# Kernel optimization log

Hardware: AMD Instinct MI355X
Metric: run time of the kernel (lower is better)

## Reference

```python
import jax, jax.numpy as jnp
import numpy as np

DIM = 64        # feature channels of x
HEADS = 4
POS_DIM = 3
NUM_IDS = 8
STR_IN = 512    # strength_linear input size
B, S, W = 4, 1024, 8   # batch, sequence (S1), source-views (S2)


def setup_inputs() -> dict:
    key = jax.random.key(0)
    ks = jax.random.split(key, 18)
    stdv = 1.0 / np.sqrt(DIM * DIM)  # embedding init per module
    d8 = DIM // 8
    u = lambda k, shp, s: jax.random.uniform(k, shp, jnp.float32, -s, s)
    return {
        "x": jax.random.normal(ks[0], (B, DIM, S, W), jnp.float32),
        "pos": jax.random.normal(ks[1], (B, S, POS_DIM), jnp.float32),
        "strength": jax.random.normal(ks[2], (STR_IN,), jnp.float32),
        "embed_id1": 3,
        "q_emb_w": u(ks[3], (NUM_IDS, DIM * DIM), stdv),
        "k_emb_w": u(ks[4], (NUM_IDS, DIM * DIM), stdv),
        "v_emb_w": u(ks[5], (NUM_IDS, DIM * DIM), stdv),
        "pos_w1": u(ks[6], (POS_DIM, POS_DIM), 1.0 / np.sqrt(POS_DIM)),
        "pos_b1": u(ks[7], (POS_DIM,), 1.0 / np.sqrt(POS_DIM)),
        "pos_w2": u(ks[8], (d8, POS_DIM), 1.0 / np.sqrt(POS_DIM)),
        "pos_b2": u(ks[9], (d8,), 1.0 / np.sqrt(POS_DIM)),
        "head_w": u(ks[10], (HEADS, d8), 1.0 / np.sqrt(d8)),
        "head_b": u(ks[11], (HEADS,), 1.0 / np.sqrt(d8)),
        "gate": jnp.ones((HEADS,), jnp.float32),
        "out_w": u(ks[12], (DIM, DIM), 1.0 / np.sqrt(DIM)),
        "out_b": u(ks[13], (DIM,), 1.0 / np.sqrt(DIM)),
        "str_w": u(ks[14], (DIM, STR_IN), 1.0 / np.sqrt(STR_IN)),
        "str_b": u(ks[15], (DIM,), 1.0 / np.sqrt(STR_IN)),
    }


def reference(x, pos, strength, embed_id1, q_emb_w, k_emb_w, v_emb_w,
              pos_w1, pos_b1, pos_w2, pos_b2, head_w, head_b, gate,
              out_w, out_b, str_w, str_b):
    # strength projection: Linear(512, dim)
    s = strength @ str_w.T + str_b                    # [dim]
    xt = jnp.transpose(x, (0, 2, 3, 1))               # [B, S, W, dim]
    qe = q_emb_w[embed_id1].reshape(DIM, DIM)
    ke = k_emb_w[embed_id1].reshape(DIM, DIM)
    ve = v_emb_w[embed_id1].reshape(DIM, DIM)

    def proj(emb):
        y = xt @ emb.T + s                            # [B, S, W, dim]
        # collapse (W, dim) -> (heads, head_dim), heads to axis 1
        y = y.reshape(B, S, HEADS, -1)
        return jnp.transpose(y, (0, 2, 1, 3))         # [B, H, S, hd]

    q, k, v = proj(qe), proj(ke), proj(ve)
    hd = q.shape[-1]
    attn = jax.nn.softmax(jnp.einsum("bhsd,bhtd->bhst", q, k) / np.sqrt(hd), axis=-1)

    # relative-position attention branch
    ph = jax.nn.relu(pos @ pos_w1.T + pos_b1) @ pos_w2.T + pos_b2   # [B, S, dim//8]
    diff = ph[:, :, None, :] - ph[:, None, :, :]                    # [B, S, S, dim//8]
    pos_attn = jnp.transpose(diff @ head_w.T + head_b, (0, 3, 1, 2))
    pos_attn = jax.nn.softmax(pos_attn, axis=-1)                    # [B, H, S, S]

    g = jax.nn.sigmoid(gate).reshape(1, -1, 1, 1)
    attn = (1.0 - g) * attn + g * pos_attn
    attn = attn / jnp.sum(attn, axis=-1, keepdims=True)

    out = jnp.einsum("bhst,bhtd->bhsd", attn, v)      # [B, H, S, hd]
    out = jnp.transpose(out, (0, 2, 1, 3)).reshape(B, S, W, DIM)
    return out @ out_w.T + out_b                      # [B, S, W, dim]
```

## Files before the change

kernel.cpp:

```cpp
#include <hip/hip_runtime.h>
#include <math.h>
#include <stdint.h>

#define B_ 4
#define S_ 1024
#define F_ 512
#define HD 128
#define SOFT_C 4.0f

typedef __attribute__((ext_vector_type(8))) short short8;
typedef __attribute__((ext_vector_type(4))) float f32x4;
typedef __attribute__((ext_vector_type(4))) unsigned int u32x4;
typedef __attribute__((ext_vector_type(2))) unsigned int u32x2;

__device__ __forceinline__ unsigned short f2bf(float f) {
    unsigned int u = __float_as_uint(f);
    u = (u + 0x7FFFu + ((u >> 16) & 1u)) >> 16;
    return (unsigned short)u;
}
__device__ __forceinline__ float bf2f(unsigned int s) {
    return __uint_as_float(s << 16);
}
__device__ __forceinline__ void pack_hilo(const float* v, u32x4& hi, u32x4& lo) {
    #pragma unroll
    for (int p = 0; p < 4; ++p) {
        unsigned int h0 = f2bf(v[2 * p]), h1 = f2bf(v[2 * p + 1]);
        float l0 = v[2 * p] - bf2f(h0), l1 = v[2 * p + 1] - bf2f(h1);
        hi[p] = h0 | (h1 << 16);
        lo[p] = (unsigned int)f2bf(l0) | ((unsigned int)f2bf(l1) << 16);
    }
}

__global__ __launch_bounds__(256) void k_qkv(
    const float* __restrict__ x, const int* __restrict__ embed_id,
    const float* __restrict__ qw, const float* __restrict__ kw,
    const float* __restrict__ vw,
    const float* __restrict__ strength, const float* __restrict__ str_w,
    const float* __restrict__ str_b,
    const float* __restrict__ pos, const float* __restrict__ pw1,
    const float* __restrict__ pb1, const float* __restrict__ pw2,
    const float* __restrict__ pb2, const float* __restrict__ head_w,
    unsigned short* __restrict__ yqh, unsigned short* __restrict__ ykh,
    unsigned short* __restrict__ yvt2,
    float* __restrict__ sv_g, float* __restrict__ xbar)
{
    __shared__ unsigned short whi[3][4096];
    __shared__ unsigned short wlo[3][4096];
    __shared__ float part_s[4][64];
    __shared__ float sv_s[64], svq_s[64];
    __shared__ float xr_s[4][8];
    __shared__ float red_s[4][4];
    __shared__ float inv_s[4];

    const int tid  = threadIdx.x;
    const int wv   = tid >> 6;
    const int lane = tid & 63;
    const int quad = lane >> 4;
    const int l15  = lane & 15;
    const float SCALE = 0.08838834764831845f;

    if (blockIdx.x >= 512) {
        const int bi = blockIdx.x - 512;
        const int b = bi >> 6, c = bi & 63;
        float w1_[9], b1_[3], w2_[24], b2_[8], hw_[32];
        #pragma unroll
        for (int i = 0; i < 9; ++i)  w1_[i] = pw1[i];
        #pragma unroll
        for (int i = 0; i < 3; ++i)  b1_[i] = pb1[i];
        #pragma unroll
        for (int i = 0; i < 24; ++i) w2_[i] = pw2[i];
        #pragma unroll
        for (int i = 0; i < 8; ++i)  b2_[i] = pb2[i];
        #pragma unroll
        for (int i = 0; i < 32; ++i) hw_[i] = head_w[i];

        float pv_[4][4];
        float ps[4] = {0.f, 0.f, 0.f, 0.f};
        #pragma unroll
        for (int rr = 0; rr < 4; ++rr) {
            const int s = tid * 4 + rr;
            float p0 = pos[(b * S_ + s) * 3 + 0];
            float p1 = pos[(b * S_ + s) * 3 + 1];
            float p2 = pos[(b * S_ + s) * 3 + 2];
            float h0 = fmaxf(0.f, p0 * w1_[0] + p1 * w1_[1] + p2 * w1_[2] + b1_[0]);
            float h1 = fmaxf(0.f, p0 * w1_[3] + p1 * w1_[4] + p2 * w1_[5] + b1_[1]);
            float h2 = fmaxf(0.f, p0 * w1_[6] + p1 * w1_[7] + p2 * w1_[8] + b1_[2]);
            float ph[8];
            #pragma unroll
            for (int o8 = 0; o8 < 8; ++o8)
                ph[o8] = h0 * w2_[o8 * 3] + h1 * w2_[o8 * 3 + 1]
                       + h2 * w2_[o8 * 3 + 2] + b2_[o8];
            #pragma unroll
            for (int h = 0; h < 4; ++h) {
                float A = 0.f;
                #pragma unroll
                for (int o8 = 0; o8 < 8; ++o8) A += ph[o8] * hw_[h * 8 + o8];
                pv_[rr][h] = __expf(-A - 1.0f);
                ps[h] += pv_[rr][h];
            }
        }
        #pragma unroll
        for (int h = 0; h < 4; ++h)
            #pragma unroll
            for (int off = 1; off < 64; off <<= 1)
                ps[h] += __shfl_xor(ps[h], off);
        if (lane == 0)
            #pragma unroll
            for (int h = 0; h < 4; ++h) red_s[wv][h] = ps[h];
        __syncthreads();
        if (tid < 4)
            inv_s[tid] = 1.f / (red_s[0][tid] + red_s[1][tid]
                              + red_s[2][tid] + red_s[3][tid]);
        __syncthreads();

        const float* xc = x + (size_t)b * 524288 + c * 8192;
        float acc[8] = {};
        #pragma unroll
        for (int rr = 0; rr < 4; ++rr) {
            const int s = tid * 4 + rr;
            f32x4 x0 = *(const f32x4*)(xc + s * 8);
            f32x4 x1 = *(const f32x4*)(xc + s * 8 + 4);
            float q0 = pv_[rr][0] * inv_s[0];
            float q1 = pv_[rr][1] * inv_s[1];
            float q2 = pv_[rr][2] * inv_s[2];
            float q3 = pv_[rr][3] * inv_s[3];
            acc[0] += q0 * x0[0]; acc[1] += q0 * x0[1];
            acc[2] += q1 * x0[2]; acc[3] += q1 * x0[3];
            acc[4] += q2 * x1[0]; acc[5] += q2 * x1[1];
            acc[6] += q3 * x1[2]; acc[7] += q3 * x1[3];
        }
        #pragma unroll
        for (int j = 0; j < 8; ++j)
            #pragma unroll
            for (int off = 1; off < 64; off <<= 1)
                acc[j] += __shfl_xor(acc[j], off);
        if (lane == 0)
            #pragma unroll
            for (int j = 0; j < 8; ++j) xr_s[wv][j] = acc[j];
        __syncthreads();
        if (tid < 8)
            xbar[(b * 8 + tid) * 64 + c] = xr_s[0][tid] + xr_s[1][tid]
                                         + xr_s[2][tid] + xr_s[3][tid];
        return;
    }

    const int id = embed_id[0];
    #pragma unroll
    for (int m = 0; m < 3; ++m) {
        const float* src = (m == 0 ? qw : m == 1 ? kw : vw) + id * 4096;
        const float sc = (m == 0) ? SCALE : 1.0f;
        for (int i = tid; i < 4096; i += 256) {
            float v = src[i] * sc;
            unsigned short hh = f2bf(v);
            const int r = i >> 6, cc = i & 63;
            const int off = ((r >> 4) * 2 + (cc >> 5)) * 512
                          + ((cc >> 3) & 3) * 128 + (r & 15) * 8 + (cc & 7);
            whi[m][off] = hh;
            wlo[m][off] = f2bf(v - bf2f(hh));
        }
    }
    {
        const float* wrow = str_w + lane * 512 + wv * 128;
        const float* st   = strength + wv * 128;
        float a = 0.f;
        #pragma unroll
        for (int j4 = 0; j4 < 32; ++j4) {
            f32x4 wv4 = *(const f32x4*)(wrow + j4 * 4);
            f32x4 s4  = *(const f32x4*)(st + j4 * 4);
            a += wv4[0] * s4[0] + wv4[1] * s4[1] + wv4[2] * s4[2] + wv4[3] * s4[3];
        }
        part_s[wv][lane] = a;
    }
    __syncthreads();
    if (tid < 64) {
        float v = part_s[0][tid] + part_s[1][tid] + part_s[2][tid]
                + part_s[3][tid] + str_b[tid];
        sv_s[tid]  = v;
        svq_s[tid] = v * SCALE;
        if (blockIdx.x == 0) sv_g[tid] = v;
    }
    __syncthreads();

    const int r0   = blockIdx.x * 64 + wv * 16;
    const int b    = r0 >> 13;
    const int rloc = (r0 & 8191) + l15;
    const float* xb = x + (size_t)b * 524288;

    u32x4 xhi[2], xlo[2];
    #pragma unroll
    for (int kc = 0; kc < 2; ++kc) {
        float xv[8];
        #pragma unroll
        for (int j = 0; j < 8; ++j)
            xv[j] = xb[(kc * 32 + quad * 8 + j) * 8192 + rloc];
        pack_hilo(xv, xhi[kc], xlo[kc]);
    }

    float svq_l[4], sv_l[4];
    #pragma unroll
    for (int nt = 0; nt < 4; ++nt) {
        svq_l[nt] = svq_s[nt * 16 + l15];
        sv_l[nt]  = sv_s[nt * 16 + l15];
    }
    f32x4 svA[4];
    #pragma unroll
    for (int mt = 0; mt < 4; ++mt)
        svA[mt] = *(const f32x4*)&sv_s[mt * 16 + quad * 4];

    int idxq[4];
    #pragma unroll
    for (int rr = 0; rr < 4; ++rr) {
        const int rl = quad * 4 + rr;
        const int w_ = rl & 7;
        const int s_loc = ((r0 & 8191) >> 3) + (rl >> 3);
        idxq[rr] = (b * 4 + (w_ >> 1)) * 131072 + s_loc * 128 + (w_ & 1) * 64 + l15;
    }

    const int row_g = r0 + l15;
    const int s_idx = (row_g >> 3) & 1023;
    const int w_idx = row_g & 7;
    const int bh    = b * 4 + (w_idx >> 1);
    const int dbase = (w_idx & 1) * 64;
    unsigned short* vtb = yvt2 + (size_t)bh * 131072 + (s_idx >> 6) * 8192
                        + (size_t)dbase * 64 + (s_idx & 63);

    #pragma unroll
    for (int mat = 0; mat < 2; ++mat) {
        const unsigned short* mh = whi[mat];
        const unsigned short* ml = wlo[mat];
        f32x4 acc[4] = {};
        #pragma unroll
        for (int kc = 0; kc < 2; ++kc)
            #pragma unroll
            for (int nt = 0; nt < 4; ++nt) {
                const int off = (nt * 2 + kc) * 512 + quad * 128 + l15 * 8;
                u32x4 ehi = *(const u32x4*)(mh + off);
                u32x4 elo = *(const u32x4*)(ml + off);
                acc[nt] = __builtin_amdgcn_mfma_f32_16x16x32_bf16(
                    __builtin_bit_cast(short8, xhi[kc]),
                    __builtin_bit_cast(short8, ehi), acc[nt], 0, 0, 0);
                acc[nt] = __builtin_amdgcn_mfma_f32_16x16x32_bf16(
                    __builtin_bit_cast(short8, xlo[kc]),
                    __builtin_bit_cast(short8, ehi), acc[nt], 0, 0, 0);
                acc[nt] = __builtin_amdgcn_mfma_f32_16x16x32_bf16(
                    __builtin_bit_cast(short8, xhi[kc]),
                    __builtin_bit_cast(short8, elo), acc[nt], 0, 0, 0);
            }
        unsigned short* y = (mat == 0 ? yqh : ykh);
        const float* svp = (mat == 0 ? svq_l : sv_l);
        #pragma unroll
        for (int nt = 0; nt < 4; ++nt)
            #pragma unroll
            for (int rr = 0; rr < 4; ++rr)
                y[(size_t)idxq[rr] + nt * 16] = f2bf(acc[nt][rr] + svp[nt]);
    }

    {
        const unsigned short* mh = whi[2];
        const unsigned short* ml = wlo[2];
        f32x4 acc[4] = {};
        #pragma unroll
        for (int kc = 0; kc < 2; ++kc)
            #pragma unroll
            for (int mt = 0; mt < 4; ++mt) {
                const int off = (mt * 2 + kc) * 512 + quad * 128 + l15 * 8;
                u32x4 ehi = *(const u32x4*)(mh + off);
                u32x4 elo = *(const u32x4*)(ml + off);
                acc[mt] = __builtin_amdgcn_mfma_f32_16x16x32_bf16(
                    __builtin_bit_cast(short8, ehi),
                    __builtin_bit_cast(short8, xhi[kc]), acc[mt], 0, 0, 0);
                acc[mt] = __builtin_amdgcn_mfma_f32_16x16x32_bf16(
                    __builtin_bit_cast(short8, ehi),
                    __builtin_bit_cast(short8, xlo[kc]), acc[mt], 0, 0, 0);
                acc[mt] = __builtin_amdgcn_mfma_f32_16x16x32_bf16(
                    __builtin_bit_cast(short8, elo),
                    __builtin_bit_cast(short8, xhi[kc]), acc[mt], 0, 0, 0);
            }
        #pragma unroll
        for (int mt = 0; mt < 4; ++mt)
            #pragma unroll
            for (int rr = 0; rr < 4; ++rr) {
                const int c = mt * 16 + quad * 4 + rr;
                vtb[(size_t)c * 64] = f2bf(acc[mt][rr] + svA[mt][rr]);
            }
    }
}

__global__ __launch_bounds__(256, 2) void k_attn(
    const unsigned short* __restrict__ yqh, const unsigned short* __restrict__ ykh,
    const unsigned short* __restrict__ yvt2,
    const float* __restrict__ xbar, const float* __restrict__ vw,
    const int* __restrict__ embed_id, const float* __restrict__ sv,
    const float* __restrict__ gate,
    const float* __restrict__ out_w, const float* __restrict__ out_b,
    float* __restrict__ out)
{
    __shared__ __align__(16) unsigned short kx[2][64 * 136];
    __shared__ __align__(16) unsigned short vx[2][128 * 72];
    __shared__ float vbar_s[128];
    __shared__ float vbarP_s[128];
    __shared__ float lsq_s[2][2][16];

    const int tid  = threadIdx.x;
    const int w    = tid >> 6;
    const int lane = tid & 63;
    const int quad = lane >> 4;
    const int l15  = lane & 15;
    const int bh = blockIdx.x & 15, qt = blockIdx.x >> 4;
    const int b = bh >> 2, h = bh & 3;
    const int s0 = qt * 32;
    const int qh = w >> 1;
    const int ts = w & 1;

    const unsigned short* ykb = ykh + (size_t)bh * 131072;
    const unsigned short* yvb = yvt2 + (size_t)bh * 131072;

    if (tid < 128) {
        const int c = tid & 63, wloc = tid >> 6;
        const float* ver = vw + embed_id[0] * 4096 + c * 64;
        const float* xbr = xbar + (b * 8 + h * 2 + wloc) * 64;
        float a = sv[c];
        #pragma unroll
        for (int j4 = 0; j4 < 16; ++j4) {
            f32x4 e4 = *(const f32x4*)(ver + j4 * 4);
            f32x4 x4 = *(const f32x4*)(xbr + j4 * 4);
            a += e4[0] * x4[0] + e4[1] * x4[1] + e4[2] * x4[2] + e4[3] * x4[3];
        }
        vbar_s[wloc * 64 + c] = a;
    }

    u32x4 qf[4];
    #pragma unroll
    for (int kc = 0; kc < 4; ++kc)
        qf[kc] = *(const u32x4*)(yqh + (size_t)bh * 131072
                 + (s0 + qh * 16 + l15) * 128 + kc * 32 + quad * 8);

    #pragma unroll
    for (int r = 0; r < 4; ++r) {
        const int off = r * 2048 + tid * 8;
        *(u32x4*)&kx[0][(off >> 7) * 136 + (off & 127)] =
            *(const u32x4*)(ykb + off);
        *(u32x4*)&vx[0][(off >> 6) * 72 + (off & 63)] =
            *(const u32x4*)(yvb + off);
    }
    __syncthreads();

    if (tid < 128) {
        const int seg = tid >> 6, dq = tid & 63;
        const float* wr = out_w + dq * 64;
        float a = 0.f;
        #pragma unroll
        for (int j4 = 0; j4 < 16; ++j4) {
            f32x4 w4 = *(const f32x4*)(wr + j4 * 4);
            f32x4 v4 = *(const f32x4*)&vbar_s[seg * 64 + j4 * 4];
            a += w4[0] * v4[0] + w4[1] * v4[1] + w4[2] * v4[2] + w4[3] * v4[3];
        }
        vbarP_s[seg * 64 + dq] = a;
    }

    f32x4 o[8] = {};
    float lsum = 0.f;
    const int srcA = ((quad & 1) << 5) + l15;

    for (int it = 0; it < 16; ++it) {
        const int cur = it & 1;
        u32x4 kst[4], vst[4];
        const bool pre = (it < 15);
        if (pre) {
            const unsigned short* ksrc = ykb + (it + 1) * 8192;
            const unsigned short* vsrc = yvb + (it + 1) * 8192;
            #pragma unroll
            for (int r = 0; r < 4; ++r)
                kst[r] = *(const u32x4*)(ksrc + r * 2048 + tid * 8);
            #pragma unroll
            for (int r = 0; r < 4; ++r)
                vst[r] = *(const u32x4*)(vsrc + r * 2048 + tid * 8);
        }

        const unsigned short* kxc = kx[cur];
        const unsigned short* vxc = vx[cur];

        f32x4 sa0 = {}, sa1 = {};
        #pragma unroll
        for (int kc = 0; kc < 4; ++kc) {
            u32x4 a0 = *(const u32x4*)&kxc[(ts * 32 + l15) * 136 + kc * 32 + quad * 8];
            sa0 = __builtin_amdgcn_mfma_f32_16x16x32_bf16(
                __builtin_bit_cast(short8, a0),
                __builtin_bit_cast(short8, qf[kc]), sa0, 0, 0, 0);
        }
        #pragma unroll
        for (int kc = 0; kc < 4; ++kc) {
            u32x4 a1 = *(const u32x4*)&kxc[(ts * 32 + 16 + l15) * 136 + kc * 32 + quad * 8];
            sa1 = __builtin_amdgcn_mfma_f32_16x16x32_bf16(
                __builtin_bit_cast(short8, a1),
                __builtin_bit_cast(short8, qf[kc]), sa1, 0, 0, 0);
        }

        float p0[4], p1[4];
        #pragma unroll
        for (int r = 0; r < 4; ++r) {
            p0[r] = __expf(sa0[r] - SOFT_C);
            p1[r] = __expf(sa1[r] - SOFT_C);
            lsum += p0[r] + p1[r];
        }

        unsigned int pk00 = (unsigned int)f2bf(p0[0]) | ((unsigned int)f2bf(p0[1]) << 16);
        unsigned int pk01 = (unsigned int)f2bf(p0[2]) | ((unsigned int)f2bf(p0[3]) << 16);
        unsigned int pk10 = (unsigned int)f2bf(p1[0]) | ((unsigned int)f2bf(p1[1]) << 16);
        unsigned int pk11 = (unsigned int)f2bf(p1[2]) | ((unsigned int)f2bf(p1[3]) << 16);
        unsigned int sel0 = (quad < 2) ? pk00 : pk10;
        unsigned int sel1 = (quad < 2) ? pk01 : pk11;
        u32x4 pf;
        pf[0] = (unsigned int)__shfl((int)sel0, srcA);
        pf[1] = (unsigned int)__shfl((int)sel1, srcA);
        pf[2] = (unsigned int)__shfl((int)sel0, srcA + 16);
        pf[3] = (unsigned int)__shfl((int)sel1, srcA + 16);

        #pragma unroll
        for (int dt = 0; dt < 8; ++dt) {
            u32x4 vf = *(const u32x4*)&vxc[(dt * 16 + l15) * 72 + ts * 32 + quad * 8];
            o[dt] = __builtin_amdgcn_mfma_f32_16x16x32_bf16(
                __builtin_bit_cast(short8, vf),
                __builtin_bit_cast(short8, pf), o[dt], 0, 0, 0);
        }

        if (pre) {
            #pragma unroll
            for (int r = 0; r < 4; ++r) {
                const int off = r * 2048 + tid * 8;
                *(u32x4*)&kx[cur ^ 1][(off >> 7) * 136 + (off & 127)] = kst[r];
            }
            #pragma unroll
            for (int r = 0; r < 4; ++r) {
                const int off = r * 2048 + tid * 8;
                *(u32x4*)&vx[cur ^ 1][(off >> 6) * 72 + (off & 63)] = vst[r];
            }
        }
        __syncthreads();
    }

    float* obuf = (float*)&kx[0][0];
    {
        float* ow_ = obuf + ((qh * 2 + ts) * 16 + l15) * 132;
        #pragma unroll
        for (int dt = 0; dt < 8; ++dt)
            *(f32x4*)(ow_ + dt * 16 + quad * 4) = o[dt];
    }
    lsum += __shfl_xor(lsum, 16);
    lsum += __shfl_xor(lsum, 32);
    if (quad == 0) lsq_s[qh][ts][l15] = lsum;
    __syncthreads();

    const float gf = 1.f / (1.f + __expf(-gate[h]));
    const float cf = (1.f - gf) / (lsq_s[qh][0][l15] + lsq_s[qh][1][l15]);
    const float* oa  = obuf + ((qh * 2 + 0) * 16 + l15) * 132;
    const float* obp = obuf + ((qh * 2 + 1) * 16 + l15) * 132;

    u32x4 bhi[2], blo[2];
    #pragma unroll
    for (int kc = 0; kc < 2; ++kc) {
        const int off = ts * 64 + kc * 32 + quad * 8;
        f32x4 a0 = *(const f32x4*)(oa + off);
        f32x4 a1 = *(const f32x4*)(oa + off + 4);
        f32x4 c0 = *(const f32x4*)(obp + off);
        f32x4 c1 = *(const f32x4*)(obp + off + 4);
        float yv[8] = {cf * (a0[0] + c0[0]), cf * (a0[1] + c0[1]),
                       cf * (a0[2] + c0[2]), cf * (a0[3] + c0[3]),
                       cf * (a1[0] + c1[0]), cf * (a1[1] + c1[1]),
                       cf * (a1[2] + c1[2]), cf * (a1[3] + c1[3])};
        pack_hilo(yv, bhi[kc], blo[kc]);
    }

    f32x4 acc[4] = {};
    #pragma unroll
    for (int kc = 0; kc < 2; ++kc)
        #pragma unroll
        for (int mt = 0; mt < 4; ++mt) {
            const float* wsrc2 = out_w + (mt * 16 + l15) * 64 + kc * 32 + quad * 8;
            f32x4 w0 = *(const f32x4*)wsrc2;
            f32x4 w1 = *(const f32x4*)(wsrc2 + 4);
            float wv8[8] = {w0[0], w0[1], w0[2], w0[3], w1[0], w1[1], w1[2], w1[3]};
            u32x4 ahi, alo;
            pack_hilo(wv8, ahi, alo);
            acc[mt] = __builtin_amdgcn_mfma_f32_16x16x32_bf16(
                __builtin_bit_cast(short8, ahi),
                __builtin_bit_cast(short8, bhi[kc]), acc[mt], 0, 0, 0);
            acc[mt] = __builtin_amdgcn_mfma_f32_16x16x32_bf16(
                __builtin_bit_cast(short8, ahi),
                __builtin_bit_cast(short8, blo[kc]), acc[mt], 0, 0, 0);
            acc[mt] = __builtin_amdgcn_mfma_f32_16x16x32_bf16(
                __builtin_bit_cast(short8, alo),
                __builtin_bit_cast(short8, bhi[kc]), acc[mt], 0, 0, 0);
        }

    const int w_seg = h * 2 + ts;
    const size_t rowb = ((size_t)(b * S_ + s0 + qh * 16 + l15) * 8 + w_seg) * 64;
    #pragma unroll
    for (int mt = 0; mt < 4; ++mt) {
        f32x4 vb   = *(const f32x4*)&vbarP_s[ts * 64 + mt * 16 + quad * 4];
        f32x4 bias = *(const f32x4*)(out_b + mt * 16 + quad * 4);
        f32x4 res;
        #pragma unroll
        for (int j = 0; j < 4; ++j) res[j] = acc[mt][j] + gf * vb[j] + bias[j];
        *(f32x4*)(out + rowb + mt * 16 + quad * 4) = res;
    }
}

extern "C" void kernel_launch(void* const* d_in, const int* in_sizes, int n_in,
                              void* d_out, int out_size, void* d_ws, size_t ws_size,
                              hipStream_t stream) {
    (void)in_sizes; (void)n_in; (void)out_size; (void)ws_size;
    const float* x        = (const float*)d_in[0];
    const float* pos      = (const float*)d_in[1];
    const float* strength = (const float*)d_in[2];
    const int*   embed_id = (const int*)d_in[3];
    const float* qw       = (const float*)d_in[4];
    const float* kw       = (const float*)d_in[5];
    const float* vw       = (const float*)d_in[6];
    const float* pw1      = (const float*)d_in[7];
    const float* pb1      = (const float*)d_in[8];
    const float* pw2      = (const float*)d_in[9];
    const float* pb2      = (const float*)d_in[10];
    const float* head_w   = (const float*)d_in[11];
    const float* gate     = (const float*)d_in[13];
    const float* out_w    = (const float*)d_in[14];
    const float* out_b    = (const float*)d_in[15];
    const float* str_w    = (const float*)d_in[16];
    const float* str_b    = (const float*)d_in[17];
    float* out = (float*)d_out;

    unsigned short* yqh   = (unsigned short*)d_ws;
    unsigned short* ykh   = yqh + 2097152;
    unsigned short* yvt2  = ykh + 2097152;
    float* sv   = (float*)(yvt2 + 2097152);
    float* xbar = sv + 64;

    k_qkv<<<768, 256, 0, stream>>>(x, embed_id, qw, kw, vw,
                                   strength, str_w, str_b,
                                   pos, pw1, pb1, pw2, pb2, head_w,
                                   yqh, ykh, yvt2, sv, xbar);
    k_attn<<<512, 256, 0, stream>>>(yqh, ykh, yvt2, xbar, vw, embed_id, sv,
                                    gate, out_w, out_b, out);
}
```

Baseline: 144.0 us.

## Fuse QKV projection and attention into one cooperative kernel with grid sync

Merges the projection kernel and the attention kernel into a single cooperative launch of 512 blocks that synchronise with a grid barrier, removing one kernel launch and the gap between launches. The separate positional/xbar blocks are folded into the projection blocks: each block computes a half-sequence xbar partial, written to two buffers that are summed later. Weight hi/lo conversion is vectorised, and launch bounds now request two blocks per CU. If the cooperative launch fails it falls back to two ordinary launches with a mode flag. The cost is a grid-wide barrier, redundant recomputation of the positional softmax sums in every block, and a larger shared allocation.

```diff
diff --git a/kernel.cpp b/kernel.cpp
--- a/kernel.cpp
+++ b/kernel.cpp
@@ -1,6 +1,9 @@
 #include <hip/hip_runtime.h>
+#include <hip/hip_cooperative_groups.h>
 #include <math.h>
 #include <stdint.h>
+
+namespace cg = cooperative_groups;
 
 #define B_ 4
 #define S_ 1024
@@ -31,26 +34,22 @@
     }
 }
 
-__global__ __launch_bounds__(256) void k_qkv(
-    const float* __restrict__ x, const int* __restrict__ embed_id,
+__global__ __launch_bounds__(256, 2) void k_fused(
+    const float* __restrict__ x, const float* __restrict__ pos,
+    const float* __restrict__ strength, const int* __restrict__ embed_id,
     const float* __restrict__ qw, const float* __restrict__ kw,
     const float* __restrict__ vw,
-    const float* __restrict__ strength, const float* __restrict__ str_w,
-    const float* __restrict__ str_b,
-    const float* __restrict__ pos, const float* __restrict__ pw1,
-    const float* __restrict__ pb1, const float* __restrict__ pw2,
-    const float* __restrict__ pb2, const float* __restrict__ head_w,
+    const float* __restrict__ pw1, const float* __restrict__ pb1,
+    const float* __restrict__ pw2, const float* __restrict__ pb2,
+    const float* __restrict__ head_w, const float* __restrict__ gate,
+    const float* __restrict__ out_w, const float* __restrict__ out_b,
+    const float* __restrict__ str_w, const float* __restrict__ str_b,
     unsigned short* __restrict__ yqh, unsigned short* __restrict__ ykh,
     unsigned short* __restrict__ yvt2,
-    float* __restrict__ sv_g, float* __restrict__ xbar)
+    float* __restrict__ sv_g, float* __restrict__ xbar0,
+    float* __restrict__ xbar1, float* __restrict__ out, int mode)
 {
-    __shared__ unsigned short whi[3][4096];
-    __shared__ unsigned short wlo[3][4096];
-    __shared__ float part_s[4][64];
-    __shared__ float sv_s[64], svq_s[64];
-    __shared__ float xr_s[4][8];
-    __shared__ float red_s[4][4];
-    __shared__ float inv_s[4];
+    __shared__ __align__(16) unsigned char smem[72960];
 
     const int tid  = threadIdx.x;
     const int wv   = tid >> 6;
@@ -59,450 +58,469 @@
     const int l15  = lane & 15;
     const float SCALE = 0.08838834764831845f;
 
-    if (blockIdx.x >= 512) {
-        const int bi = blockIdx.x - 512;
-        const int b = bi >> 6, c = bi & 63;
-        float w1_[9], b1_[3], w2_[24], b2_[8], hw_[32];
+    if (mode != 2) {
+        unsigned short* whiB = (unsigned short*)smem;
+        unsigned short* wloB = whiB + 12288;
+        float* part_s = (float*)(smem + 49152);
+        float* sv_s   = (float*)(smem + 50176);
+        float* svq_s  = (float*)(smem + 50432);
+        float* xr_s   = (float*)(smem + 50688);
+        float* red_s  = (float*)(smem + 50816);
+        float* inv_s  = (float*)(smem + 50880);
+
+        const int id = embed_id[0];
+
+        for (int cc = tid; cc < 1536; cc += 256) {
+            const int m  = cc >> 9;
+            const int e0 = (cc & 511) << 3;
+            const float* src = (m == 0 ? qw : m == 1 ? kw : vw) + id * 4096 + e0;
+            const float sc = (m == 0) ? SCALE : 1.0f;
+            f32x4 a0 = *(const f32x4*)src;
+            f32x4 a1 = *(const f32x4*)(src + 4);
+            float v8[8] = {a0[0] * sc, a0[1] * sc, a0[2] * sc, a0[3] * sc,
+                           a1[0] * sc, a1[1] * sc, a1[2] * sc, a1[3] * sc};
+            u32x4 hi, lo;
+            pack_hilo(v8, hi, lo);
+            const int r = e0 >> 6, c = e0 & 63;
+            const int off = ((r >> 4) * 2 + (c >> 5)) * 512
+                          + ((c >> 3) & 3) * 128 + (r & 15) * 8;
+            *(u32x4*)(whiB + m * 4096 + off) = hi;
+            *(u32x4*)(wloB + m * 4096 + off) = lo;
+        }
+
+        {
+            const float* wrow = str_w + lane * 512 + wv * 128;
+            const float* st   = strength + wv * 128;
+            float a = 0.f;
+            #pragma unroll
+            for (int j4 = 0; j4 < 32; ++j4) {
+                f32x4 wv4 = *(const f32x4*)(wrow + j4 * 4);
+                f32x4 s4  = *(const f32x4*)(st + j4 * 4);
+                a += wv4[0] * s4[0] + wv4[1] * s4[1] + wv4[2] * s4[2] + wv4[3] * s4[3];
+            }
+            part_s[wv * 64 + lane] = a;
+        }
+        __syncthreads();
+        if (tid < 64) {
+            float v = part_s[tid] + part_s[64 + tid] + part_s[128 + tid]
+                    + part_s[192 + tid] + str_b[tid];
+            sv_s[tid]  = v;
+            svq_s[tid] = v * SCALE;
+            if (blockIdx.x == 0) sv_g[tid] = v;
+        }
+        __syncthreads();
+
+        {
+            const int r0   = blockIdx.x * 64 + wv * 16;
+            const int b    = r0 >> 13;
+            const int rloc = (r0 & 8191) + l15;
+            const float* xb = x + (size_t)b * 524288;
+
+            u32x4 xhi[2], xlo[2];
+            #pragma unroll
+            for (int kc = 0; kc < 2; ++kc) {
+                float xv[8];
+                #pragma unroll
+                for (int j = 0; j < 8; ++j)
+                    xv[j] = xb[(kc * 32 + quad * 8 + j) * 8192 + rloc];
+                pack_hilo(xv, xhi[kc], xlo[kc]);
+            }
+
+            float svq_l[4], sv_l[4];
+            #pragma unroll
+            for (int nt = 0; nt < 4; ++nt) {
+                svq_l[nt] = svq_s[nt * 16 + l15];
+                sv_l[nt]  = sv_s[nt * 16 + l15];
+            }
+            f32x4 svA[4];
+            #pragma unroll
+            for (int mt = 0; mt < 4; ++mt)
+                svA[mt] = *(const f32x4*)&sv_s[mt * 16 + quad * 4];
+
+            int idxq[4];
+            #pragma unroll
+            for (int rr = 0; rr < 4; ++rr) {
+                const int rl = quad * 4 + rr;
+                const int w_ = rl & 7;
+                const int s_loc = ((r0 & 8191) >> 3) + (rl >> 3);
+                idxq[rr] = (b * 4 + (w_ >> 1)) * 131072 + s_loc * 128 + (w_ & 1) * 64 + l15;
+            }
+
+            const int row_g = r0 + l15;
+            const int s_idx = (row_g >> 3) & 1023;
+            const int w_idx = row_g & 7;
+            const int bh    = b * 4 + (w_idx >> 1);
+            const int dbase = (w_idx & 1) * 64;
+            unsigned short* vtb = yvt2 + (size_t)bh * 131072 + (s_idx >> 6) * 8192
+                                + (size_t)dbase * 64 + (s_idx & 63);
+
+            #pragma unroll
+            for (int mat = 0; mat < 2; ++mat) {
+                const unsigned short* mh = whiB + mat * 4096;
+                const unsigned short* ml = wloB + mat * 4096;
+                f32x4 acc[4] = {};
+                #pragma unroll
+                for (int kc = 0; kc < 2; ++kc)
+                    #pragma unroll
+                    for (int nt = 0; nt < 4; ++nt) {
+                        const int off = (nt * 2 + kc) * 512 + quad * 128 + l15 * 8;
+                        u32x4 ehi = *(const u32x4*)(mh + off);
+                        u32x4 elo = *(const u32x4*)(ml + off);
+                        acc[nt] = __builtin_amdgcn_mfma_f32_16x16x32_bf16(
+                            __builtin_bit_cast(short8, xhi[kc]),
+                            __builtin_bit_cast(short8, ehi), acc[nt], 0, 0, 0);
+                        acc[nt] = __builtin_amdgcn_mfma_f32_16x16x32_bf16(
+                            __builtin_bit_cast(short8, xlo[kc]),
+                            __builtin_bit_cast(short8, ehi), acc[nt], 0, 0, 0);
+                        acc[nt] = __builtin_amdgcn_mfma_f32_16x16x32_bf16(
+                            __builtin_bit_cast(short8, xhi[kc]),
+                            __builtin_bit_cast(short8, elo), acc[nt], 0, 0, 0);
+                    }
+                unsigned short* y = (mat == 0 ? yqh : ykh);
+                const float* svp = (mat == 0 ? svq_l : sv_l);
+                #pragma unroll
+                for (int nt = 0; nt < 4; ++nt)
+                    #pragma unroll
+                    for (int rr = 0; rr < 4; ++rr)
+                        y[(size_t)idxq[rr] + nt * 16] = f2bf(acc[nt][rr] + svp[nt]);
+            }
+
+            {
+                const unsigned short* mh = whiB + 2 * 4096;
+                const unsigned short* ml = wloB + 2 * 4096;
+                f32x4 acc[4] = {};
+                #pragma unroll
+                for (int kc = 0; kc < 2; ++kc)
+                    #pragma unroll
+                    for (int mt = 0; mt < 4; ++mt) {
+                        const int off = (mt * 2 + kc) * 512 + quad * 128 + l15 * 8;
+                        u32x4 ehi = *(const u32x4*)(mh + off);
+                        u32x4 elo = *(const u32x4*)(ml + off);
+                        acc[mt] = __builtin_amdgcn_mfma_f32_16x16x32_bf16(
+                            __builtin_bit_cast(short8, ehi),
+                            __builtin_bit_cast(short8, xhi[kc]), acc[mt], 0, 0, 0);
+                        acc[mt] = __builtin_amdgcn_mfma_f32_16x16x32_bf16(
+                            __builtin_bit_cast(short8, ehi),
+                            __builtin_bit_cast(short8, xlo[kc]), acc[mt], 0, 0, 0);
+                        acc[mt] = __builtin_amdgcn_mfma_f32_16x16x32_bf16(
+                            __builtin_bit_cast(short8, elo),
+                            __builtin_bit_cast(short8, xhi[kc]), acc[mt], 0, 0, 0);
+                    }
+                #pragma unroll
+                for (int mt = 0; mt < 4; ++mt)
+                    #pragma unroll
+                    for (int rr = 0; rr < 4; ++rr) {
+                        const int c = mt * 16 + quad * 4 + rr;
+                        vtb[(size_t)c * 64] = f2bf(acc[mt][rr] + svA[mt][rr]);
+                    }
+            }
+        }
+
+        {
+            const int g  = blockIdx.x;
+            const int xh = g >> 8, bi = g & 255;
+            const int bb = bi >> 6, c = bi & 63;
+
+            float w1_[9], b1_[3], w2_[24], b2_[8], hw_[32];
+            #pragma unroll
+            for (int i = 0; i < 9; ++i)  w1_[i] = pw1[i];
+            #pragma unroll
+            for (int i = 0; i < 3; ++i)  b1_[i] = pb1[i];
+            #pragma unroll
+            for (int i = 0; i < 24; ++i) w2_[i] = pw2[i];
+            #pragma unroll
+            for (int i = 0; i < 8; ++i)  b2_[i] = pb2[i];
+            #pragma unroll
+            for (int i = 0; i < 32; ++i) hw_[i] = head_w[i];
+
+            float evh[2][4];
+            float ps[4] = {0.f, 0.f, 0.f, 0.f};
+            #pragma unroll
+            for (int k = 0; k < 4; ++k) {
+                const int s = k * 256 + tid;
+                float p0 = pos[(bb * S_ + s) * 3 + 0];
+                float p1 = pos[(bb * S_ + s) * 3 + 1];
+                float p2 = pos[(bb * S_ + s) * 3 + 2];
+                float h0 = fmaxf(0.f, p0 * w1_[0] + p1 * w1_[1] + p2 * w1_[2] + b1_[0]);
+                float h1 = fmaxf(0.f, p0 * w1_[3] + p1 * w1_[4] + p2 * w1_[5] + b1_[1]);
+                float h2 = fmaxf(0.f, p0 * w1_[6] + p1 * w1_[7] + p2 * w1_[8] + b1_[2]);
+                float ph[8];
+                #pragma unroll
+                for (int o8 = 0; o8 < 8; ++o8)
+                    ph[o8] = h0 * w2_[o8 * 3] + h1 * w2_[o8 * 3 + 1]
+                           + h2 * w2_[o8 * 3 + 2] + b2_[o8];
+                #pragma unroll
+                for (int h = 0; h < 4; ++h) {
+                    float A = 0.f;
+                    #pragma unroll
+                    for (int o8 = 0; o8 < 8; ++o8) A += ph[o8] * hw_[h * 8 + o8];
+                    float e = __expf(-A - 1.0f);
+                    ps[h] += e;
+                    if ((k >> 1) == xh) evh[k & 1][h] = e;
+                }
+            }
+            #pragma unroll
+            for (int h = 0; h < 4; ++h)
+                #pragma unroll
+                for (int off = 1; off < 64; off <<= 1)
+                    ps[h] += __shfl_xor(ps[h], off);
+            if (lane == 0)
+                #pragma unroll
+                for (int h = 0; h < 4; ++h) red_s[wv * 4 + h] = ps[h];
+            __syncthreads();
+            if (tid < 4)
+                inv_s[tid] = 1.f / (red_s[tid] + red_s[4 + tid]
+                                  + red_s[8 + tid] + red_s[12 + tid]);
+            __syncthreads();
+
+            const float* xc = x + (size_t)bb * 524288 + c * 8192;
+            float acc[8] = {};
+            #pragma unroll
+            for (int kk = 0; kk < 2; ++kk) {
+                const int s = (xh * 2 + kk) * 256 + tid;
+                f32x4 x0 = *(const f32x4*)(xc + s * 8);
+                f32x4 x1 = *(const f32x4*)(xc + s * 8 + 4);
+                float q0 = evh[kk][0] * inv_s[0];
+                float q1 = evh[kk][1] * inv_s[1];
+                float q2 = evh[kk][2] * inv_s[2];
+                float q3 = evh[kk][3] * inv_s[3];
+                acc[0] += q0 * x0[0]; acc[1] += q0 * x0[1];
+                acc[2] += q1 * x0[2]; acc[3] += q1 * x0[3];
+                acc[4] += q2 * x1[0]; acc[5] += q2 * x1[1];
+                acc[6] += q3 * x1[2]; acc[7] += q3 * x1[3];
+            }
+            #pragma unroll
+            for (int j = 0; j < 8; ++j)
+                #pragma unroll
+                for (int off = 1; off < 64; off <<= 1)
+                    acc[j] += __shfl_xor(acc[j], off);
+            if (lane == 0)
+                #pragma unroll
+                for (int j = 0; j < 8; ++j) xr_s[wv * 8 + j] = acc[j];
+            __syncthreads();
+            if (tid < 8) {
+                float* xb_h = xh ? xbar1 : xbar0;
+                xb_h[(bb * 8 + tid) * 64 + c] = xr_s[tid] + xr_s[8 + tid]
+                                              + xr_s[16 + tid] + xr_s[24 + tid];
+            }
+        }
+
+        if (mode == 1) return;
+        __threadfence();
+        cg::this_grid().sync();
+    }
+
+    {
+        unsigned short* kxb = (unsigned short*)smem;
+        unsigned short* vxb = (unsigned short*)(smem + 34816);
+        float* vbar_s  = (float*)(smem + 71680);
+        float* vbarP_s = (float*)(smem + 72192);
+        float* lsq_s   = (float*)(smem + 72704);
+
+        const int bh = blockIdx.x & 15, qt = blockIdx.x >> 4;
+        const int b = bh >> 2, h = bh & 3;
+        const int s0 = qt * 32;
+        const int qh = wv >> 1;
+        const int ts = wv & 1;
+
+        const unsigned short* ykb = ykh + (size_t)bh * 131072;
+        const unsigned short* yvb = yvt2 + (size_t)bh * 131072;
+
+        if (tid < 128) {
+            const int c = tid & 63, wloc = tid >> 6;
+            const float* ver = vw + embed_id[0] * 4096 + c * 64;
+            const float* xr0 = xbar0 + (b * 8 + h * 2 + wloc) * 64;
+            const float* xr1 = xbar1 + (b * 8 + h * 2 + wloc) * 64;
+            float a = sv_g[c];
+            #pragma unroll
+            for (int j4 = 0; j4 < 16; ++j4) {
+                f32x4 e4 = *(const f32x4*)(ver + j4 * 4);
+                f32x4 xa = *(const f32x4*)(xr0 + j4 * 4);
+                f32x4 xb4 = *(const f32x4*)(xr1 + j4 * 4);
+                a += e4[0] * (xa[0] + xb4[0]) + e4[1] * (xa[1] + xb4[1])
+                   + e4[2] * (xa[2] + xb4[2]) + e4[3] * (xa[3] + xb4[3]);
+            }
+            vbar_s[wloc * 64 + c] = a;
+        }
+
+        u32x4 qf[4];
         #pragma unroll
-        for (int i = 0; i < 9; ++i)  w1_[i] = pw1[i];
+        for (int kc = 0; kc < 4; ++kc)
+            qf[kc] = *(const u32x4*)(yqh + (size_t)bh * 131072
+                     + (s0 + qh * 16 + l15) * 128 + kc * 32 + quad * 8);
+
         #pragma unroll
-        for (int i = 0; i < 3; ++i)  b1_[i] = pb1[i];
+        for (int r = 0; r < 4; ++r) {
+            const int off = r * 2048 + tid * 8;
+            *(u32x4*)(kxb + (off >> 7) * 136 + (off & 127)) =
+                *(const u32x4*)(ykb + off);
+            *(u32x4*)(vxb + (off >> 6) * 72 + (off & 63)) =
+                *(const u32x4*)(yvb + off);
+        }
+        __syncthreads();
+
+        if (tid < 128) {
+            const int seg = tid >> 6, dq = tid & 63;
+            const float* wr = out_w + dq * 64;
+            float a = 0.f;
+            #pragma unroll
+            for (int j4 = 0; j4 < 16; ++j4) {
+                f32x4 w4 = *(const f32x4*)(wr + j4 * 4);
+                f32x4 v4 = *(const f32x4*)&vbar_s[seg * 64 + j4 * 4];
+                a += w4[0] * v4[0] + w4[1] * v4[1] + w4[2] * v4[2] + w4[3] * v4[3];
+            }
+            vbarP_s[seg * 64 + dq] = a;
+        }
+
+        f32x4 o[8] = {};
+        float lsum = 0.f;
+        const int srcA = ((quad & 1) << 5) + l15;
+
+        for (int it = 0; it < 16; ++it) {
+            const int cur = it & 1;
+            u32x4 kst[4], vst[4];
+            const bool pre = (it < 15);
+            if (pre) {
+                const unsigned short* ksrc = ykb + (it + 1) * 8192;
+                const unsigned short* vsrc = yvb + (it + 1) * 8192;
+                #pragma unroll
+                for (int r = 0; r < 4; ++r)
+                    kst[r] = *(const u32x4*)(ksrc + r * 2048 + tid * 8);
+                #pragma unroll
+                for (int r = 0; r < 4; ++r)
+                    vst[r] = *(const u32x4*)(vsrc + r * 2048 + tid * 8);
+            }
+
+            const unsigned short* kxc = kxb + cur * 8704;
+            const unsigned short* vxc = vxb + cur * 9216;
+
+            f32x4 sa0 = {}, sa1 = {};
+            #pragma unroll
+            for (int kc = 0; kc < 4; ++kc) {
+                u32x4 a0 = *(const u32x4*)&kxc[(ts * 32 + l15) * 136 + kc * 32 + quad * 8];
+                sa0 = __builtin_amdgcn_mfma_f32_16x16x32_bf16(
+                    __builtin_bit_cast(short8, a0),
+                    __builtin_bit_cast(short8, qf[kc]), sa0, 0, 0, 0);
+            }
+            #pragma unroll
+            for (int kc = 0; kc < 4; ++kc) {
+                u32x4 a1 = *(const u32x4*)&kxc[(ts * 32 + 16 + l15) * 136 + kc * 32 + quad * 8];
+                sa1 = __builtin_amdgcn_mfma_f32_16x16x32_bf16(
+                    __builtin_bit_cast(short8, a1),
+                    __builtin_bit_cast(short8, qf[kc]), sa1, 0, 0, 0);
+            }
+
+            float p0[4], p1[4];
+            #pragma unroll
+            for (int r = 0; r < 4; ++r) {
+                p0[r] = __expf(sa0[r] - SOFT_C);
+                p1[r] = __expf(sa1[r] - SOFT_C);
+                lsum += p0[r] + p1[r];
+            }
+
+            unsigned int pk00 = (unsigned int)f2bf(p0[0]) | ((unsigned int)f2bf(p0[1]) << 16);
+            unsigned int pk01 = (unsigned int)f2bf(p0[2]) | ((unsigned int)f2bf(p0[3]) << 16);
+            unsigned int pk10 = (unsigned int)f2bf(p1[0]) | ((unsigned int)f2bf(p1[1]) << 16);
+            unsigned int pk11 = (unsigned int)f2bf(p1[2]) | ((unsigned int)f2bf(p1[3]) << 16);
+            unsigned int sel0 = (quad < 2) ? pk00 : pk10;
+            unsigned int sel1 = (quad < 2) ? pk01 : pk11;
+            u32x4 pf;
+            pf[0] = (unsigned int)__shfl((int)sel0, srcA);
+            pf[1] = (unsigned int)__shfl((int)sel1, srcA);
+            pf[2] = (unsigned int)__shfl((int)sel0, srcA + 16);
+            pf[3] = (unsigned int)__shfl((int)sel1, srcA + 16);
+
+            #pragma unroll
+            for (int dt = 0; dt < 8; ++dt) {
+                u32x4 vf = *(const u32x4*)&vxc[(dt * 16 + l15) * 72 + ts * 32 + quad * 8];
+                o[dt] = __builtin_amdgcn_mfma_f32_16x16x32_bf16(
+                    __builtin_bit_cast(short8, vf),
+                    __builtin_bit_cast(short8, pf), o[dt], 0, 0, 0);
+            }
+
+            if (pre) {
+                unsigned short* kxn = kxb + (cur ^ 1) * 8704;
+                unsigned short* vxn = vxb + (cur ^ 1) * 9216;
+                #pragma unroll
+                for (int r = 0; r < 4; ++r) {
+                    const int off = r * 2048 + tid * 8;
+                    *(u32x4*)(kxn + (off >> 7) * 136 + (off & 127)) = kst[r];
+                }
+                #pragma unroll
+                for (int r = 0; r < 4; ++r) {
+                    const int off = r * 2048 + tid * 8;
+                    *(u32x4*)(vxn + (off >> 6) * 72 + (off & 63)) = vst[r];
+                }
+            }
+            __syncthreads();
+        }
+
+        float* obuf = (float*)smem;
+        {
+            float* ow_ = obuf + ((qh * 2 + ts) * 16 + l15) * 132;
+            #pragma unroll
+            for (int dt = 0; dt < 8; ++dt)
+                *(f32x4*)(ow_ + dt * 16 + quad * 4) = o[dt];
+        }
+        lsum += __shfl_xor(lsum, 16);
+        lsum += __shfl_xor(lsum, 32);
+        if (quad == 0) lsq_s[(qh * 2 + ts) * 16 + l15] = lsum;
+        __syncthreads();
+
+        const float gf = 1.f / (1.f + __expf(-gate[h]));
+        const float cf = (1.f - gf) / (lsq_s[(qh * 2) * 16 + l15]
+                                     + lsq_s[(qh * 2 + 1) * 16 + l15]);
+        const float* oa  = obuf + ((qh * 2 + 0) * 16 + l15) * 132;
+        const float* obp = obuf + ((qh * 2 + 1) * 16 + l15) * 132;
+
+        u32x4 bhi[2], blo[2];
         #pragma unroll
-        for (int i = 0; i < 24; ++i) w2_[i] = pw2[i];
-        #pragma unroll
-        for (int i = 0; i < 8; ++i)  b2_[i] = pb2[i];
-        #pragma unroll
-        for (int i = 0; i < 32; ++i) hw_[i] = head_w[i];
-
-        float pv_[4][4];
-        float ps[4] = {0.f, 0.f, 0.f, 0.f};
-        #pragma unroll
-        for (int rr = 0; rr < 4; ++rr) {
-            const int s = tid * 4 + rr;
-            float p0 = pos[(b * S_ + s) * 3 + 0];
-            float p1 = pos[(b * S_ + s) * 3 + 1];
-            float p2 = pos[(b * S_ + s) * 3 + 2];
-            float h0 = fmaxf(0.f, p0 * w1_[0] + p1 * w1_[1] + p2 * w1_[2] + b1_[0]);
-            float h1 = fmaxf(0.f, p0 * w1_[3] + p1 * w1_[4] + p2 * w1_[5] + b1_[1]);
-            float h2 = fmaxf(0.f, p0 * w1_[6] + p1 * w1_[7] + p2 * w1_[8] + b1_[2]);
-            float ph[8];
-            #pragma unroll
-            for (int o8 = 0; o8 < 8; ++o8)
-                ph[o8] = h0 * w2_[o8 * 3] + h1 * w2_[o8 * 3 + 1]
-                       + h2 * w2_[o8 * 3 + 2] + b2_[o8];
-            #pragma unroll
-            for (int h = 0; h < 4; ++h) {
-                float A = 0.f;
-                #pragma unroll
-                for (int o8 = 0; o8 < 8; ++o8) A += ph[o8] * hw_[h * 8 + o8];
-                pv_[rr][h] = __expf(-A - 1.0f);
-                ps[h] += pv_[rr][h];
-            }
-        }
-        #pragma unroll
-        for (int h = 0; h < 4; ++h)
-            #pragma unroll
-            for (int off = 1; off < 64; off <<= 1)
-                ps[h] += __shfl_xor(ps[h], off);
-        if (lane == 0)
-            #pragma unroll
-            for (int h = 0; h < 4; ++h) red_s[wv][h] = ps[h];
-        __syncthreads();
-        if (tid < 4)
-            inv_s[tid] = 1.f / (red_s[0][tid] + red_s[1][tid]
-                              + red_s[2][tid] + red_s[3][tid]);
-        __syncthreads();
-
-        const float* xc = x + (size_t)b * 524288 + c * 8192;
-        float acc[8] = {};
-        #pragma unroll
-        for (int rr = 0; rr < 4; ++rr) {
-            const int s = tid * 4 + rr;
-            f32x4 x0 = *(const f32x4*)(xc + s * 8);
-            f32x4 x1 = *(const f32x4*)(xc + s * 8 + 4);
-            float q0 = pv_[rr][0] * inv_s[0];
-            float q1 = pv_[rr][1] * inv_s[1];
-            float q2 = pv_[rr][2] * inv_s[2];
-            float q3 = pv_[rr][3] * inv_s[3];
-            acc[0] += q0 * x0[0]; acc[1] += q0 * x0[1];
-            acc[2] += q1 * x0[2]; acc[3] += q1 * x0[3];
-            acc[4] += q2 * x1[0]; acc[5] += q2 * x1[1];
-            acc[6] += q3 * x1[2]; acc[7] += q3 * x1[3];
-        }
-        #pragma unroll
-        for (int j = 0; j < 8; ++j)
-            #pragma unroll
-            for (int off = 1; off < 64; off <<= 1)
-                acc[j] += __shfl_xor(acc[j], off);
-        if (lane == 0)
-            #pragma unroll
-            for (int j = 0; j < 8; ++j) xr_s[wv][j] = acc[j];
-        __syncthreads();
-        if (tid < 8)
-            xbar[(b * 8 + tid) * 64 + c] = xr_s[0][tid] + xr_s[1][tid]
-                                         + xr_s[2][tid] + xr_s[3][tid];
-        return;
-    }
-
-    const int id = embed_id[0];
-    #pragma unroll
-    for (int m = 0; m < 3; ++m) {
-        const float* src = (m == 0 ? qw : m == 1 ? kw : vw) + id * 4096;
-        const float sc = (m == 0) ? SCALE : 1.0f;
-        for (int i = tid; i < 4096; i += 256) {
-            float v = src[i] * sc;
-            unsigned short hh = f2bf(v);
-            const int r = i >> 6, cc = i & 63;
-            const int off = ((r >> 4) * 2 + (cc >> 5)) * 512
-                          + ((cc >> 3) & 3) * 128 + (r & 15) * 8 + (cc & 7);
-            whi[m][off] = hh;
-            wlo[m][off] = f2bf(v - bf2f(hh));
-        }
-    }
-    {
-        const float* wrow = str_w + lane * 512 + wv * 128;
-        const float* st   = strength + wv * 128;
-        float a = 0.f;
-        #pragma unroll
-        for (int j4 = 0; j4 < 32; ++j4) {
-            f32x4 wv4 = *(const f32x4*)(wrow + j4 * 4);
-            f32x4 s4  = *(const f32x4*)(st + j4 * 4);
-            a += wv4[0] * s4[0] + wv4[1] * s4[1] + wv4[2] * s4[2] + wv4[3] * s4[3];
-        }
-        part_s[wv][lane] = a;
-    }
-    __syncthreads();
-    if (tid < 64) {
-        float v = part_s[0][tid] + part_s[1][tid] + part_s[2][tid]
-                + part_s[3][tid] + str_b[tid];
-        sv_s[tid]  = v;
-        svq_s[tid] = v * SCALE;
-        if (blockIdx.x == 0) sv_g[tid] = v;
-    }
-    __syncthreads();
-
-    const int r0   = blockIdx.x * 64 + wv * 16;
-    const int b    = r0 >> 13;
-    const int rloc = (r0 & 8191) + l15;
-    const float* xb = x + (size_t)b * 524288;
-
-    u32x4 xhi[2], xlo[2];
-    #pragma unroll
-    for (int kc = 0; kc < 2; ++kc) {
-        float xv[8];
-        #pragma unroll
-        for (int j = 0; j < 8; ++j)
-            xv[j] = xb[(kc * 32 + quad * 8 + j) * 8192 + rloc];
-        pack_hilo(xv, xhi[kc], xlo[kc]);
-    }
-
-    float svq_l[4], sv_l[4];
-    #pragma unroll
-    for (int nt = 0; nt < 4; ++nt) {
-        svq_l[nt] = svq_s[nt * 16 + l15];
-        sv_l[nt]  = sv_s[nt * 16 + l15];
-    }
-    f32x4 svA[4];
-    #pragma unroll
-    for (int mt = 0; mt < 4; ++mt)
-        svA[mt] = *(const f32x4*)&sv_s[mt * 16 + quad * 4];
-
-    int idxq[4];
-    #pragma unroll
-    for (int rr = 0; rr < 4; ++rr) {
-        const int rl = quad * 4 + rr;
-        const int w_ = rl & 7;
-        const int s_loc = ((r0 & 8191) >> 3) + (rl >> 3);
-        idxq[rr] = (b * 4 + (w_ >> 1)) * 131072 + s_loc * 128 + (w_ & 1) * 64 + l15;
-    }
-
-    const int row_g = r0 + l15;
-    const int s_idx = (row_g >> 3) & 1023;
-    const int w_idx = row_g & 7;
-    const int bh    = b * 4 + (w_idx >> 1);
-    const int dbase = (w_idx & 1) * 64;
-    unsigned short* vtb = yvt2 + (size_t)bh * 131072 + (s_idx >> 6) * 8192
-                        + (size_t)dbase * 64 + (s_idx & 63);
-
-    #pragma unroll
-    for (int mat = 0; mat < 2; ++mat) {
-        const unsigned short* mh = whi[mat];
-        const unsigned short* ml = wlo[mat];
+        for (int kc = 0; kc < 2; ++kc) {
+            const int off = ts * 64 + kc * 32 + quad * 8;
+            f32x4 a0 = *(const f32x4*)(oa + off);
+            f32x4 a1 = *(const f32x4*)(oa + off + 4);
+            f32x4 c0 = *(const f32x4*)(obp + off);
+            f32x4 c1 = *(const f32x4*)(obp + off + 4);
+            float yv[8] = {cf * (a0[0] + c0[0]), cf * (a0[1] + c0[1]),
+                           cf * (a0[2] + c0[2]), cf * (a0[3] + c0[3]),
+                           cf * (a1[0] + c1[0]), cf * (a1[1] + c1[1]),
+                           cf * (a1[2] + c1[2]), cf * (a1[3] + c1[3])};
+            pack_hilo(yv, bhi[kc], blo[kc]);
+        }
+
         f32x4 acc[4] = {};
         #pragma unroll
         for (int kc = 0; kc < 2; ++kc)
             #pragma unroll
-            for (int nt = 0; nt < 4; ++nt) {
-                const int off = (nt * 2 + kc) * 512 + quad * 128 + l15 * 8;
-                u32x4 ehi = *(const u32x4*)(mh + off);
-                u32x4 elo = *(const u32x4*)(ml + off);
-                acc[nt] = __builtin_amdgcn_mfma_f32_16x16x32_bf16(
-                    __builtin_bit_cast(short8, xhi[kc]),
-                    __builtin_bit_cast(short8, ehi), acc[nt], 0, 0, 0);
-                acc[nt] = __builtin_amdgcn_mfma_f32_16x16x32_bf16(
-                    __builtin_bit_cast(short8, xlo[kc]),
-                    __builtin_bit_cast(short8, ehi), acc[nt], 0, 0, 0);
-                acc[nt] = __builtin_amdgcn_mfma_f32_16x16x32_bf16(
-                    __builtin_bit_cast(short8, xhi[kc]),
-                    __builtin_bit_cast(short8, elo), acc[nt], 0, 0, 0);
-            }
-        unsigned short* y = (mat == 0 ? yqh : ykh);
-        const float* svp = (mat == 0 ? svq_l : sv_l);
-        #pragma unroll
-        for (int nt = 0; nt < 4; ++nt)
-            #pragma unroll
-            for (int rr = 0; rr < 4; ++rr)
-                y[(size_t)idxq[rr] + nt * 16] = f2bf(acc[nt][rr] + svp[nt]);
-    }
-
-    {
-        const unsigned short* mh = whi[2];
-        const unsigned short* ml = wlo[2];
-        f32x4 acc[4] = {};
-        #pragma unroll
-        for (int kc = 0; kc < 2; ++kc)
-            #pragma unroll
             for (int mt = 0; mt < 4; ++mt) {
-                const int off = (mt * 2 + kc) * 512 + quad * 128 + l15 * 8;
-                u32x4 ehi = *(const u32x4*)(mh + off);
-                u32x4 elo = *(const u32x4*)(ml + off);
+                const float* wsrc2 = out_w + (mt * 16 + l15) * 64 + kc * 32 + quad * 8;
+                f32x4 w0 = *(const f32x4*)wsrc2;
+                f32x4 w1 = *(const f32x4*)(wsrc2 + 4);
+                float wv8[8] = {w0[0], w0[1], w0[2], w0[3], w1[0], w1[1], w1[2], w1[3]};
+                u32x4 ahi, alo;
+                pack_hilo(wv8, ahi, alo);
                 acc[mt] = __builtin_amdgcn_mfma_f32_16x16x32_bf16(
-                    __builtin_bit_cast(short8, ehi),
-                    __builtin_bit_cast(short8, xhi[kc]), acc[mt], 0, 0, 0);
+                    __builtin_bit_cast(short8, ahi),
+                    __builtin_bit_cast(short8, bhi[kc]), acc[mt], 0, 0, 0);
                 acc[mt] = __builtin_amdgcn_mfma_f32_16x16x32_bf16(
-                    __builtin_bit_cast(short8, ehi),
-                    __builtin_bit_cast(short8, xlo[kc]), acc[mt], 0, 0, 0);
+                    __builtin_bit_cast(short8, ahi),
+                    __builtin_bit_cast(short8, blo[kc]), acc[mt], 0, 0, 0);
                 acc[mt] = __builtin_amdgcn_mfma_f32_16x16x32_bf16(
-                    __builtin_bit_cast(short8, elo),
-                    __builtin_bit_cast(short8, xhi[kc]), acc[mt], 0, 0, 0);
-            }
-        #pragma unroll
-        for (int mt = 0; mt < 4; ++mt)
-            #pragma unroll
-            for (int rr = 0; rr < 4; ++rr) {
-                const int c = mt * 16 + quad * 4 + rr;
-                vtb[(size_t)c * 64] = f2bf(acc[mt][rr] + svA[mt][rr]);
-            }
-    }
-}
-
-__global__ __launch_bounds__(256, 2) void k_attn(
-    const unsigned short* __restrict__ yqh, const unsigned short* __restrict__ ykh,
-    const unsigned short* __restrict__ yvt2,
-    const float* __restrict__ xbar, const float* __restrict__ vw,
-    const int* __restrict__ embed_id, const float* __restrict__ sv,
-    const float* __restrict__ gate,
-    const float* __restrict__ out_w, const float* __restrict__ out_b,
-    float* __restrict__ out)
-{
-    __shared__ __align__(16) unsigned short kx[2][64 * 136];
-    __shared__ __align__(16) unsigned short vx[2][128 * 72];
-    __shared__ float vbar_s[128];
-    __shared__ float vbarP_s[128];
-    __shared__ float lsq_s[2][2][16];
-
-    const int tid  = threadIdx.x;
-    const int w    = tid >> 6;
-    const int lane = tid & 63;
-    const int quad = lane >> 4;
-    const int l15  = lane & 15;
-    const int bh = blockIdx.x & 15, qt = blockIdx.x >> 4;
-    const int b = bh >> 2, h = bh & 3;
-    const int s0 = qt * 32;
-    const int qh = w >> 1;
-    const int ts = w & 1;
-
-    const unsigned short* ykb = ykh + (size_t)bh * 131072;
-    const unsigned short* yvb = yvt2 + (size_t)bh * 131072;
-
-    if (tid < 128) {
-        const int c = tid & 63, wloc = tid >> 6;
-        const float* ver = vw + embed_id[0] * 4096 + c * 64;
-        const float* xbr = xbar + (b * 8 + h * 2 + wloc) * 64;
-        float a = sv[c];
-        #pragma unroll
-        for (int j4 = 0; j4 < 16; ++j4) {
-            f32x4 e4 = *(const f32x4*)(ver + j4 * 4);
-            f32x4 x4 = *(const f32x4*)(xbr + j4 * 4);
-            a += e4[0] * x4[0] + e4[1] * x4[1] + e4[2] * x4[2] + e4[3] * x4[3];
-        }
-        vbar_s[wloc * 64 + c] = a;
-    }
-
-    u32x4 qf[4];
-    #pragma unroll
-    for (int kc = 0; kc < 4; ++kc)
-        qf[kc] = *(const u32x4*)(yqh + (size_t)bh * 131072
-                 + (s0 + qh * 16 + l15) * 128 + kc * 32 + quad * 8);
-
-    #pragma unroll
-    for (int r = 0; r < 4; ++r) {
-        const int off = r * 2048 + tid * 8;
-        *(u32x4*)&kx[0][(off >> 7) * 136 + (off & 127)] =
-            *(const u32x4*)(ykb + off);
-        *(u32x4*)&vx[0][(off >> 6) * 72 + (off & 63)] =
-            *(const u32x4*)(yvb + off);
-    }
-    __syncthreads();
-
-    if (tid < 128) {
-        const int seg = tid >> 6, dq = tid & 63;
-        const float* wr = out_w + dq * 64;
-        float a = 0.f;
-        #pragma unroll
-        for (int j4 = 0; j4 < 16; ++j4) {
-            f32x4 w4 = *(const f32x4*)(wr + j4 * 4);
-            f32x4 v4 = *(const f32x4*)&vbar_s[seg * 64 + j4 * 4];
-            a += w4[0] * v4[0] + w4[1] * v4[1] + w4[2] * v4[2] + w4[3] * v4[3];
-        }
-        vbarP_s[seg * 64 + dq] = a;
-    }
-
-    f32x4 o[8] = {};
-    float lsum = 0.f;
-    const int srcA = ((quad & 1) << 5) + l15;
-
-    for (int it = 0; it < 16; ++it) {
-        const int cur = it & 1;
-        u32x4 kst[4], vst[4];
-        const bool pre = (it < 15);
-        if (pre) {
-            const unsigned short* ksrc = ykb + (it + 1) * 8192;
-            const unsigned short* vsrc = yvb + (it + 1) * 8192;
-            #pragma unroll
-            for (int r = 0; r < 4; ++r)
-                kst[r] = *(const u32x4*)(ksrc + r * 2048 + tid * 8);
-            #pragma unroll
-            for (int r = 0; r < 4; ++r)
-                vst[r] = *(const u32x4*)(vsrc + r * 2048 + tid * 8);
-        }
-
-        const unsigned short* kxc = kx[cur];
-        const unsigned short* vxc = vx[cur];
-
-        f32x4 sa0 = {}, sa1 = {};
-        #pragma unroll
-        for (int kc = 0; kc < 4; ++kc) {
-            u32x4 a0 = *(const u32x4*)&kxc[(ts * 32 + l15) * 136 + kc * 32 + quad * 8];
-            sa0 = __builtin_amdgcn_mfma_f32_16x16x32_bf16(
-                __builtin_bit_cast(short8, a0),
-                __builtin_bit_cast(short8, qf[kc]), sa0, 0, 0, 0);
-        }
-        #pragma unroll
-        for (int kc = 0; kc < 4; ++kc) {
-            u32x4 a1 = *(const u32x4*)&kxc[(ts * 32 + 16 + l15) * 136 + kc * 32 + quad * 8];
-            sa1 = __builtin_amdgcn_mfma_f32_16x16x32_bf16(
-                __builtin_bit_cast(short8, a1),
-                __builtin_bit_cast(short8, qf[kc]), sa1, 0, 0, 0);
-        }
-
-        float p0[4], p1[4];
-        #pragma unroll
-        for (int r = 0; r < 4; ++r) {
-            p0[r] = __expf(sa0[r] - SOFT_C);
-            p1[r] = __expf(sa1[r] - SOFT_C);
-            lsum += p0[r] + p1[r];
-        }
-
-        unsigned int pk00 = (unsigned int)f2bf(p0[0]) | ((unsigned int)f2bf(p0[1]) << 16);
-        unsigned int pk01 = (unsigned int)f2bf(p0[2]) | ((unsigned int)f2bf(p0[3]) << 16);
-        unsigned int pk10 = (unsigned int)f2bf(p1[0]) | ((unsigned int)f2bf(p1[1]) << 16);
-        unsigned int pk11 = (unsigned int)f2bf(p1[2]) | ((unsigned int)f2bf(p1[3]) << 16);
-        unsigned int sel0 = (quad < 2) ? pk00 : pk10;
-        unsigned int sel1 = (quad < 2) ? pk01 : pk11;
-        u32x4 pf;
-        pf[0] = (unsigned int)__shfl((int)sel0, srcA);
-        pf[1] = (unsigned int)__shfl((int)sel1, srcA);
-        pf[2] = (unsigned int)__shfl((int)sel0, srcA + 16);
-        pf[3] = (unsigned int)__shfl((int)sel1, srcA + 16);
-
-        #pragma unroll
-        for (int dt = 0; dt < 8; ++dt) {
-            u32x4 vf = *(const u32x4*)&vxc[(dt * 16 + l15) * 72 + ts * 32 + quad * 8];
-            o[dt] = __builtin_amdgcn_mfma_f32_16x16x32_bf16(
-                __builtin_bit_cast(short8, vf),
-                __builtin_bit_cast(short8, pf), o[dt], 0, 0, 0);
-        }
-
-        if (pre) {
-            #pragma unroll
-            for (int r = 0; r < 4; ++r) {
-                const int off = r * 2048 + tid * 8;
-                *(u32x4*)&kx[cur ^ 1][(off >> 7) * 136 + (off & 127)] = kst[r];
-            }
-            #pragma unroll
-            for (int r = 0; r < 4; ++r) {
-                const int off = r * 2048 + tid * 8;
-                *(u32x4*)&vx[cur ^ 1][(off >> 6) * 72 + (off & 63)] = vst[r];
-            }
-        }
-        __syncthreads();
-    }
-
-    float* obuf = (float*)&kx[0][0];
-    {
-        float* ow_ = obuf + ((qh * 2 + ts) * 16 + l15) * 132;
-        #pragma unroll
-        for (int dt = 0; dt < 8; ++dt)
-            *(f32x4*)(ow_ + dt * 16 + quad * 4) = o[dt];
-    }
-    lsum += __shfl_xor(lsum, 16);
-    lsum += __shfl_xor(lsum, 32);
-    if (quad == 0) lsq_s[qh][ts][l15] = lsum;
-    __syncthreads();
-
-    const float gf = 1.f / (1.f + __expf(-gate[h]));
-    const float cf = (1.f - gf) / (lsq_s[qh][0][l15] + lsq_s[qh][1][l15]);
-    const float* oa  = obuf + ((qh * 2 + 0) * 16 + l15) * 132;
-    const float* obp = obuf + ((qh * 2 + 1) * 16 + l15) * 132;
-
-    u32x4 bhi[2], blo[2];
-    #pragma unroll
-    for (int kc = 0; kc < 2; ++kc) {
-        const int off = ts * 64 + kc * 32 + quad * 8;
-        f32x4 a0 = *(const f32x4*)(oa + off);
-        f32x4 a1 = *(const f32x4*)(oa + off + 4);
-        f32x4 c0 = *(const f32x4*)(obp + off);
-        f32x4 c1 = *(const f32x4*)(obp + off + 4);
-        float yv[8] = {cf * (a0[0] + c0[0]), cf * (a0[1] + c0[1]),
-                       cf * (a0[2] + c0[2]), cf * (a0[3] + c0[3]),
-                       cf * (a1[0] + c1[0]), cf * (a1[1] + c1[1]),
-                       cf * (a1[2] + c1[2]), cf * (a1[3] + c1[3])};
-        pack_hilo(yv, bhi[kc], blo[kc]);
-    }
-
-    f32x4 acc[4] = {};
-    #pragma unroll
-    for (int kc = 0; kc < 2; ++kc)
+                    __builtin_bit_cast(short8, alo),
+                    __builtin_bit_cast(short8, bhi[kc]), acc[mt], 0, 0, 0);
+            }
+
+        const int w_seg = h * 2 + ts;
+        const size_t rowb = ((size_t)(b * S_ + s0 + qh * 16 + l15) * 8 + w_seg) * 64;
         #pragma unroll
         for (int mt = 0; mt < 4; ++mt) {
-            const float* wsrc2 = out_w + (mt * 16 + l15) * 64 + kc * 32 + quad * 8;
-            f32x4 w0 = *(const f32x4*)wsrc2;
-            f32x4 w1 = *(const f32x4*)(wsrc2 + 4);
-            float wv8[8] = {w0[0], w0[1], w0[2], w0[3], w1[0], w1[1], w1[2], w1[3]};
-            u32x4 ahi, alo;
-            pack_hilo(wv8, ahi, alo);
-            acc[mt] = __builtin_amdgcn_mfma_f32_16x16x32_bf16(
-                __builtin_bit_cast(short8, ahi),
-                __builtin_bit_cast(short8, bhi[kc]), acc[mt], 0, 0, 0);
-            acc[mt] = __builtin_amdgcn_mfma_f32_16x16x32_bf16(
-                __builtin_bit_cast(short8, ahi),
-                __builtin_bit_cast(short8, blo[kc]), acc[mt], 0, 0, 0);
-            acc[mt] = __builtin_amdgcn_mfma_f32_16x16x32_bf16(
-                __builtin_bit_cast(short8, alo),
-                __builtin_bit_cast(short8, bhi[kc]), acc[mt], 0, 0, 0);
-        }
-
-    const int w_seg = h * 2 + ts;
-    const size_t rowb = ((size_t)(b * S_ + s0 + qh * 16 + l15) * 8 + w_seg) * 64;
-    #pragma unroll
-    for (int mt = 0; mt < 4; ++mt) {
-        f32x4 vb   = *(const f32x4*)&vbarP_s[ts * 64 + mt * 16 + quad * 4];
-        f32x4 bias = *(const f32x4*)(out_b + mt * 16 + quad * 4);
-        f32x4 res;
-        #pragma unroll
-        for (int j = 0; j < 4; ++j) res[j] = acc[mt][j] + gf * vb[j] + bias[j];
-        *(f32x4*)(out + rowb + mt * 16 + quad * 4) = res;
+            f32x4 vb   = *(const f32x4*)&vbarP_s[ts * 64 + mt * 16 + quad * 4];
+            f32x4 bias = *(const f32x4*)(out_b + mt * 16 + quad * 4);
+            f32x4 res;
+            #pragma unroll
+            for (int j = 0; j < 4; ++j) res[j] = acc[mt][j] + gf * vb[j] + bias[j];
+            *(f32x4*)(out + rowb + mt * 16 + quad * 4) = res;
+        }
     }
 }
 
@@ -532,13 +550,30 @@
     unsigned short* yqh   = (unsigned short*)d_ws;
     unsigned short* ykh   = yqh + 2097152;
     unsigned short* yvt2  = ykh + 2097152;
-    float* sv   = (float*)(yvt2 + 2097152);
-    float* xbar = sv + 64;
-
-    k_qkv<<<768, 256, 0, stream>>>(x, embed_id, qw, kw, vw,
-                                   strength, str_w, str_b,
-                                   pos, pw1, pb1, pw2, pb2, head_w,
-                                   yqh, ykh, yvt2, sv, xbar);
-    k_attn<<<512, 256, 0, stream>>>(yqh, ykh, yvt2, xbar, vw, embed_id, sv,
-                                    gate, out_w, out_b, out);
+    float* sv    = (float*)(yvt2 + 2097152);
+    float* xbar0 = sv + 64;
+    float* xbar1 = xbar0 + 2048;
+
+    int mode0 = 0;
+    void* kargs[] = { (void*)&x, (void*)&pos, (void*)&strength, (void*)&embed_id,
+                      (void*)&qw, (void*)&kw, (void*)&vw,
+                      (void*)&pw1, (void*)&pb1, (void*)&pw2, (void*)&pb2,
+                      (void*)&head_w, (void*)&gate, (void*)&out_w, (void*)&out_b,
+                      (void*)&str_w, (void*)&str_b,
+                      (void*)&yqh, (void*)&ykh, (void*)&yvt2,
+                      (void*)&sv, (void*)&xbar0, (void*)&xbar1,
+                      (void*)&out, (void*)&mode0 };
+
+    hipError_t e = hipLaunchCooperativeKernel(
+        reinterpret_cast<void*>(&k_fused), dim3(512), dim3(256), kargs, 0, stream);
+    if (e != hipSuccess) {
+        k_fused<<<512, 256, 0, stream>>>(x, pos, strength, embed_id, qw, kw, vw,
+                                         pw1, pb1, pw2, pb2, head_w, gate,
+                                         out_w, out_b, str_w, str_b,
+                                         yqh, ykh, yvt2, sv, xbar0, xbar1, out, 1);
+        k_fused<<<512, 256, 0, stream>>>(x, pos, strength, embed_id, qw, kw, vw,
+                                         pw1, pb1, pw2, pb2, head_w, gate,
+                                         out_w, out_b, str_w, str_b,
+                                         yqh, ykh, yvt2, sv, xbar0, xbar1, out, 2);
+    }
 }
```

Measured after the change: 293.3 us. 2.04x slower.
